# Performance work log

Hardware: AMD Instinct MI355X
Metric: run time of the kernel (lower is better)

Reference implementation:

```python
import jax, jax.numpy as jnp
import numpy as np

THR = 1.0        # snntorch Leaky default threshold
SLOPE = 25.0     # fast_sigmoid default slope
NUM_STEPS = 15
BETAS = (0.9, 0.88, 0.86, 0.84, 0.82)

@jax.custom_vjp
def fire(mem):
    # Heaviside forward, fast_sigmoid surrogate backward
    return (mem > THR).astype(mem.dtype)

def _fire_fwd(mem):
    return fire(mem), mem

def _fire_bwd(mem, g):
    return (g / (SLOPE * jnp.abs(mem - THR) + 1.0) ** 2,)

fire.defvjp(_fire_fwd, _fire_bwd)

def lif(cur, mem, beta):
    # snntorch Leaky, reset_mechanism='subtract': reset computed from PREVIOUS mem
    reset = jax.lax.stop_gradient((mem > THR).astype(cur.dtype))
    mem_new = beta * mem + cur - reset * THR
    spk = fire(mem_new)
    return spk, mem_new

def setup_inputs() -> dict:
    key = jax.random.key(0)
    ks = jax.random.split(key, 13)
    B = 16384
    dims = [(256, 6), (256, 256), (256, 256), (256, 256), (128, 256), (3, 128)]
    inp = {"x": jax.random.normal(ks[0], (B, 6), dtype=jnp.float32)}
    for i, (o, fin) in enumerate(dims):
        s = 1.0 / np.sqrt(fin)
        inp[f"W{i+1}"] = jax.random.uniform(ks[1 + 2 * i], (o, fin), jnp.float32, -s, s)
        inp[f"b{i+1}"] = jax.random.uniform(ks[2 + 2 * i], (o,), jnp.float32, -s, s)
    return inp

def reference(x, W1, b1, W2, b2, W3, b3, W4, b4, W5, b5, W6, b6):
    B = x.shape[0]
    cur1 = x @ W1.T + b1  # input is constant across timesteps
    mems0 = (jnp.zeros((B, 256), x.dtype), jnp.zeros((B, 256), x.dtype),
             jnp.zeros((B, 256), x.dtype), jnp.zeros((B, 256), x.dtype),
             jnp.zeros((B, 128), x.dtype))

    def step(carry, _):
        (m1, m2, m3, m4, m5), acc = carry
        spk1, m1 = lif(cur1, m1, BETAS[0])
        spk2, m2 = lif(spk1 @ W2.T + b2, m2, BETAS[1])
        spk3, m3 = lif(spk2 @ W3.T + b3, m3, BETAS[2])
        spk4, m4 = lif(spk3 @ W4.T + b4, m4, BETAS[3])
        spk5, m5 = lif(spk4 @ W5.T + b5, m5, BETAS[4])
        out = spk5 @ W6.T + b6
        return ((m1, m2, m3, m4, m5), acc + out), None

    (_, out_sum), _ = jax.lax.scan(step, (mems0, jnp.zeros((B, 3), x.dtype)),
                                   None, length=NUM_STEPS)
    return out_sum / NUM_STEPS
```

## Files before the change

kernel.cpp:

```cpp
#include <hip/hip_runtime.h>

#define B_SZ 16384

__global__ __launch_bounds__(256) void k_transpose(const float* __restrict__ src,
                                                   float* __restrict__ dst,
                                                   int R, int C) {
    __shared__ float tile[32][33];
    int bx = blockIdx.x * 32, by = blockIdx.y * 32;
    int tx = threadIdx.x & 31, ty = threadIdx.x >> 5;
#pragma unroll
    for (int r = ty; r < 32; r += 8) {
        int gr = by + r, gc = bx + tx;
        if (gr < R && gc < C) tile[r][tx] = src[gr * C + gc];
    }
    __syncthreads();
#pragma unroll
    for (int r = ty; r < 32; r += 8) {
        int gr = bx + r, gc = by + tx;
        if (gr < C && gc < R) dst[gr * R + gc] = tile[tx][r];
    }
}

__device__ __forceinline__ void mm256(const float* __restrict__ WT,
                                      const float (*slds)[16],
                                      const int* flagrow, int q, int g0,
                                      float* acc) {
#pragma unroll
    for (int k = 0; k < 16; ++k) acc[k] = 0.f;
    int4 f = *(const int4*)flagrow;
    if ((f.x | f.y | f.z | f.w) == 0) return;
    const float4* wp = (const float4*)WT + q;
#pragma unroll 4
    for (int i = 0; i < 256; ++i) {
        float4 w4 = wp[i * 64];
        float4 s4 = *(const float4*)&slds[i][g0];
        acc[0]  = fmaf(s4.x, w4.x, acc[0]);
        acc[1]  = fmaf(s4.y, w4.x, acc[1]);
        acc[2]  = fmaf(s4.z, w4.x, acc[2]);
        acc[3]  = fmaf(s4.w, w4.x, acc[3]);
        acc[4]  = fmaf(s4.x, w4.y, acc[4]);
        acc[5]  = fmaf(s4.y, w4.y, acc[5]);
        acc[6]  = fmaf(s4.z, w4.y, acc[6]);
        acc[7]  = fmaf(s4.w, w4.y, acc[7]);
        acc[8]  = fmaf(s4.x, w4.z, acc[8]);
        acc[9]  = fmaf(s4.y, w4.z, acc[9]);
        acc[10] = fmaf(s4.z, w4.z, acc[10]);
        acc[11] = fmaf(s4.w, w4.z, acc[11]);
        acc[12] = fmaf(s4.x, w4.w, acc[12]);
        acc[13] = fmaf(s4.y, w4.w, acc[13]);
        acc[14] = fmaf(s4.z, w4.w, acc[14]);
        acc[15] = fmaf(s4.w, w4.w, acc[15]);
    }
}

__device__ __forceinline__ int lif4x4(float* m, const float* acc, const float* b4,
                                      float beta, float (*slds)[16], int j0, int g0) {
    int any = 0;
#pragma unroll
    for (int jj = 0; jj < 4; ++jj) {
        float4 sp;
#pragma unroll
        for (int gg = 0; gg < 4; ++gg) {
            int k = jj * 4 + gg;
            float cur = acc[k] + b4[jj];
            float mp  = m[k];
            float mn  = fmaf(beta, mp, cur) - (mp > 1.f ? 1.f : 0.f);
            m[k] = mn;
            int s1 = (mn > 1.f);
            any |= s1;
            ((float*)&sp)[gg] = s1 ? 1.f : 0.f;
        }
        *(float4*)&slds[j0 + jj][g0] = sp;
    }
    return any;
}

__global__ __launch_bounds__(256, 3) void k_snn(
    const float* __restrict__ x,   const float* __restrict__ W1, const float* __restrict__ b1,
    const float* __restrict__ Wt2, const float* __restrict__ b2,
    const float* __restrict__ Wt3, const float* __restrict__ b3,
    const float* __restrict__ Wt4, const float* __restrict__ b4,
    const float* __restrict__ Wt5, const float* __restrict__ b5,
    const float* __restrict__ W6,  const float* __restrict__ b6,
    float* __restrict__ out)
{
    __shared__ __align__(16) float slds[256][16];
    __shared__ float w6l[3][128];
    __shared__ float xl[16][8];
    __shared__ __align__(16) int flags[5][4];

    const int t    = threadIdx.x;
    const int s0   = blockIdx.x * 16;
    const int q    = t >> 2, r = t & 3;
    const int j0   = q * 4, g0 = r * 4;
    const int lane = t & 63, wvid = t >> 6;

    for (int k = t; k < 384; k += 256) ((float*)w6l)[k] = W6[k];
    if (t < 128) { int g = t >> 3, c = t & 7; xl[g][c] = (c < 6) ? x[(s0 + g) * 6 + c] : 0.f; }
    __syncthreads();

    const float4 b2q = *(const float4*)&b2[j0];
    const float4 b3q = *(const float4*)&b3[j0];
    const float4 b4q = *(const float4*)&b4[j0];
    const float2 b5q = *(const float2*)&b5[q * 2];
    const int og = t / 3, ok = t - og * 3;
    const float b6v = (t < 48) ? b6[ok] : 0.f;

    float cur1[16];
#pragma unroll
    for (int jj = 0; jj < 4; ++jj) {
        float w1r[6];
#pragma unroll
        for (int k = 0; k < 6; ++k) w1r[k] = W1[(j0 + jj) * 6 + k];
        float bb = b1[j0 + jj];
#pragma unroll
        for (int gg = 0; gg < 4; ++gg) {
            float s = 0.f;
#pragma unroll
            for (int k = 0; k < 6; ++k) s = fmaf(xl[g0 + gg][k], w1r[k], s);
            cur1[jj * 4 + gg] = s + bb;
        }
    }

    float m1[16], m2[16], m3[16], m4[16], m5[8], acc[16];
#pragma unroll
    for (int k = 0; k < 16; ++k) { m1[k] = 0.f; m2[k] = 0.f; m3[k] = 0.f; m4[k] = 0.f; }
#pragma unroll
    for (int k = 0; k < 8; ++k) m5[k] = 0.f;
    float accout = 0.f;
    const float zb[4] = {0.f, 0.f, 0.f, 0.f};

#pragma unroll 1
    for (int step = 0; step < 15; ++step) {
        __syncthreads();

        {
            int any = lif4x4(m1, cur1, zb, 0.9f, slds, j0, g0);
            unsigned long long bl = __ballot(any);
            if (lane == 0) flags[0][wvid] = (bl != 0ULL) ? 1 : 0;
        }
        __syncthreads();

        mm256(Wt2, slds, &flags[0][0], q, g0, acc);
        __syncthreads();
        {
            int any = lif4x4(m2, acc, (const float*)&b2q, 0.88f, slds, j0, g0);
            unsigned long long bl = __ballot(any);
            if (lane == 0) flags[1][wvid] = (bl != 0ULL) ? 1 : 0;
        }
        __syncthreads();

        mm256(Wt3, slds, &flags[1][0], q, g0, acc);
        __syncthreads();
        {
            int any = lif4x4(m3, acc, (const float*)&b3q, 0.86f, slds, j0, g0);
            unsigned long long bl = __ballot(any);
            if (lane == 0) flags[2][wvid] = (bl != 0ULL) ? 1 : 0;
        }
        __syncthreads();

        mm256(Wt4, slds, &flags[2][0], q, g0, acc);
        __syncthreads();
        {
            int any = lif4x4(m4, acc, (const float*)&b4q, 0.84f, slds, j0, g0);
            unsigned long long bl = __ballot(any);
            if (lane == 0) flags[3][wvid] = (bl != 0ULL) ? 1 : 0;
        }
        __syncthreads();

        {
            float acc5[8];
#pragma unroll
            for (int k = 0; k < 8; ++k) acc5[k] = 0.f;
            int4 f = *(const int4*)&flags[3][0];
            if (f.x | f.y | f.z | f.w) {
                const float2* wp5 = (const float2*)Wt5 + q;
#pragma unroll 4
                for (int i = 0; i < 256; ++i) {
                    float2 w2 = wp5[i * 64];
                    float4 s4 = *(const float4*)&slds[i][g0];
                    acc5[0] = fmaf(s4.x, w2.x, acc5[0]);
                    acc5[1] = fmaf(s4.y, w2.x, acc5[1]);
                    acc5[2] = fmaf(s4.z, w2.x, acc5[2]);
                    acc5[3] = fmaf(s4.w, w2.x, acc5[3]);
                    acc5[4] = fmaf(s4.x, w2.y, acc5[4]);
                    acc5[5] = fmaf(s4.y, w2.y, acc5[5]);
                    acc5[6] = fmaf(s4.z, w2.y, acc5[6]);
                    acc5[7] = fmaf(s4.w, w2.y, acc5[7]);
                }
            }
            __syncthreads();
            int any = 0;
#pragma unroll
            for (int jj = 0; jj < 2; ++jj) {
                float4 sp;
#pragma unroll
                for (int gg = 0; gg < 4; ++gg) {
                    int k = jj * 4 + gg;
                    float cur = acc5[k] + ((const float*)&b5q)[jj];
                    float mp  = m5[k];
                    float mn  = fmaf(0.82f, mp, cur) - (mp > 1.f ? 1.f : 0.f);
                    m5[k] = mn;
                    int s1 = (mn > 1.f);
                    any |= s1;
                    ((float*)&sp)[gg] = s1 ? 1.f : 0.f;
                }
                *(float4*)&slds[q * 2 + jj][g0] = sp;
            }
            unsigned long long bl = __ballot(any);
            if (lane == 0) flags[4][wvid] = (bl != 0ULL) ? 1 : 0;
        }
        __syncthreads();

        {
            int4 f = *(const int4*)&flags[4][0];
            if (t < 48) {
                float ov = b6v;
                if (f.x | f.y | f.z | f.w) {
                    float s = 0.f;
#pragma unroll 4
                    for (int i = 0; i < 128; ++i) s = fmaf(slds[i][og], w6l[ok][i], s);
                    ov = s + b6v;
                }
                accout += ov;
            }
        }
    }

    if (t < 48) out[(s0 + og) * 3 + ok] = accout / 15.0f;
}

extern "C" void kernel_launch(void* const* d_in, const int* in_sizes, int n_in,
                              void* d_out, int out_size, void* d_ws, size_t ws_size,
                              hipStream_t stream) {
    const float* x  = (const float*)d_in[0];
    const float* W1 = (const float*)d_in[1];
    const float* b1 = (const float*)d_in[2];
    const float* W2 = (const float*)d_in[3];
    const float* b2 = (const float*)d_in[4];
    const float* W3 = (const float*)d_in[5];
    const float* b3 = (const float*)d_in[6];
    const float* W4 = (const float*)d_in[7];
    const float* b4 = (const float*)d_in[8];
    const float* W5 = (const float*)d_in[9];
    const float* b5 = (const float*)d_in[10];
    const float* W6 = (const float*)d_in[11];
    const float* b6 = (const float*)d_in[12];
    float* out = (float*)d_out;

    float* ws  = (float*)d_ws;
    float* Wt2 = ws;
    float* Wt3 = Wt2 + 65536;
    float* Wt4 = Wt3 + 65536;
    float* Wt5 = Wt4 + 65536;
    size_t need = (size_t)(65536 * 3 + 32768) * sizeof(float);
    if (ws_size < need) return;

    k_transpose<<<dim3(8, 8), 256, 0, stream>>>(W2, Wt2, 256, 256);
    k_transpose<<<dim3(8, 8), 256, 0, stream>>>(W3, Wt3, 256, 256);
    k_transpose<<<dim3(8, 8), 256, 0, stream>>>(W4, Wt4, 256, 256);
    k_transpose<<<dim3(8, 4), 256, 0, stream>>>(W5, Wt5, 128, 256);
    k_snn<<<B_SZ / 16, 256, 0, stream>>>(x, W1, b1, Wt2, b2, Wt3, b3,
                                         Wt4, b4, Wt5, b5, W6, b6, out);
}
```

Measured before the change: 2.640 ms.

## Ping-pong spike buffers to drop barriers and retile to 8 neurons x 2 samples

Spikes now go into two alternating LDS buffers, so each layer writes one buffer while the next matmul reads the other. This removes the barrier that separated each matmul from the following LIF write, leaving about five block syncs per timestep instead of eleven. Each thread now computes 8 output neurons for 2 samples instead of 4 for 4. Weights are read as two float4s per row across paired input rows, against a k-pair interleaved spike layout. The cost is double the spike LDS footprint and more complex indexing, which may change bank-conflict behaviour and register pressure.

```diff
diff --git a/kernel.cpp b/kernel.cpp
--- a/kernel.cpp
+++ b/kernel.cpp
@@ -21,56 +21,119 @@
     }
 }
 
-__device__ __forceinline__ void mm256(const float* __restrict__ WT,
-                                      const float (*slds)[16],
-                                      const int* flagrow, int q, int g0,
-                                      float* acc) {
+
+__device__ __forceinline__ void mm256_8x2(const float* __restrict__ WT,
+                                          const float (*sp)[16][2],
+                                          const int* flagrow, int q, int r,
+                                          float* acc) {
 #pragma unroll
     for (int k = 0; k < 16; ++k) acc[k] = 0.f;
     int4 f = *(const int4*)flagrow;
     if ((f.x | f.y | f.z | f.w) == 0) return;
-    const float4* wp = (const float4*)WT + q;
-#pragma unroll 4
-    for (int i = 0; i < 256; ++i) {
-        float4 w4 = wp[i * 64];
-        float4 s4 = *(const float4*)&slds[i][g0];
-        acc[0]  = fmaf(s4.x, w4.x, acc[0]);
-        acc[1]  = fmaf(s4.y, w4.x, acc[1]);
-        acc[2]  = fmaf(s4.z, w4.x, acc[2]);
-        acc[3]  = fmaf(s4.w, w4.x, acc[3]);
-        acc[4]  = fmaf(s4.x, w4.y, acc[4]);
-        acc[5]  = fmaf(s4.y, w4.y, acc[5]);
-        acc[6]  = fmaf(s4.z, w4.y, acc[6]);
-        acc[7]  = fmaf(s4.w, w4.y, acc[7]);
-        acc[8]  = fmaf(s4.x, w4.z, acc[8]);
-        acc[9]  = fmaf(s4.y, w4.z, acc[9]);
-        acc[10] = fmaf(s4.z, w4.z, acc[10]);
-        acc[11] = fmaf(s4.w, w4.z, acc[11]);
-        acc[12] = fmaf(s4.x, w4.w, acc[12]);
-        acc[13] = fmaf(s4.y, w4.w, acc[13]);
-        acc[14] = fmaf(s4.z, w4.w, acc[14]);
-        acc[15] = fmaf(s4.w, w4.w, acc[15]);
-    }
-}
-
-__device__ __forceinline__ int lif4x4(float* m, const float* acc, const float* b4,
-                                      float beta, float (*slds)[16], int j0, int g0) {
+#pragma unroll 2
+    for (int ip = 0; ip < 128; ++ip) {
+        float4 s4 = *(const float4*)&sp[ip][r * 2][0];
+        const float* w0 = WT + (2 * ip) * 256 + q * 8;
+        float4 wa0 = *(const float4*)(w0);
+        float4 wa1 = *(const float4*)(w0 + 4);
+        float4 wb0 = *(const float4*)(w0 + 256);
+        float4 wb1 = *(const float4*)(w0 + 260);
+        acc[0]  = fmaf(s4.x, wa0.x, acc[0]);  acc[0]  = fmaf(s4.y, wb0.x, acc[0]);
+        acc[1]  = fmaf(s4.z, wa0.x, acc[1]);  acc[1]  = fmaf(s4.w, wb0.x, acc[1]);
+        acc[2]  = fmaf(s4.x, wa0.y, acc[2]);  acc[2]  = fmaf(s4.y, wb0.y, acc[2]);
+        acc[3]  = fmaf(s4.z, wa0.y, acc[3]);  acc[3]  = fmaf(s4.w, wb0.y, acc[3]);
+        acc[4]  = fmaf(s4.x, wa0.z, acc[4]);  acc[4]  = fmaf(s4.y, wb0.z, acc[4]);
+        acc[5]  = fmaf(s4.z, wa0.z, acc[5]);  acc[5]  = fmaf(s4.w, wb0.z, acc[5]);
+        acc[6]  = fmaf(s4.x, wa0.w, acc[6]);  acc[6]  = fmaf(s4.y, wb0.w, acc[6]);
+        acc[7]  = fmaf(s4.z, wa0.w, acc[7]);  acc[7]  = fmaf(s4.w, wb0.w, acc[7]);
+        acc[8]  = fmaf(s4.x, wa1.x, acc[8]);  acc[8]  = fmaf(s4.y, wb1.x, acc[8]);
+        acc[9]  = fmaf(s4.z, wa1.x, acc[9]);  acc[9]  = fmaf(s4.w, wb1.x, acc[9]);
+        acc[10] = fmaf(s4.x, wa1.y, acc[10]); acc[10] = fmaf(s4.y, wb1.y, acc[10]);
+        acc[11] = fmaf(s4.z, wa1.y, acc[11]); acc[11] = fmaf(s4.w, wb1.y, acc[11]);
+        acc[12] = fmaf(s4.x, wa1.z, acc[12]); acc[12] = fmaf(s4.y, wb1.z, acc[12]);
+        acc[13] = fmaf(s4.z, wa1.z, acc[13]); acc[13] = fmaf(s4.w, wb1.z, acc[13]);
+        acc[14] = fmaf(s4.x, wa1.w, acc[14]); acc[14] = fmaf(s4.y, wb1.w, acc[14]);
+        acc[15] = fmaf(s4.z, wa1.w, acc[15]); acc[15] = fmaf(s4.w, wb1.w, acc[15]);
+    }
+}
+
+__device__ __forceinline__ void mm128_4x2(const float* __restrict__ WT5,
+                                          const float (*sp)[16][2],
+                                          const int* flagrow, int q, int r,
+                                          float* acc) {
+#pragma unroll
+    for (int k = 0; k < 8; ++k) acc[k] = 0.f;
+    int4 f = *(const int4*)flagrow;
+    if ((f.x | f.y | f.z | f.w) == 0) return;
+#pragma unroll 2
+    for (int ip = 0; ip < 128; ++ip) {
+        float4 s4 = *(const float4*)&sp[ip][r * 2][0];
+        const float* w0 = WT5 + (2 * ip) * 128 + q * 4;
+        float4 wa = *(const float4*)(w0);
+        float4 wb = *(const float4*)(w0 + 128);
+        acc[0] = fmaf(s4.x, wa.x, acc[0]); acc[0] = fmaf(s4.y, wb.x, acc[0]);
+        acc[1] = fmaf(s4.z, wa.x, acc[1]); acc[1] = fmaf(s4.w, wb.x, acc[1]);
+        acc[2] = fmaf(s4.x, wa.y, acc[2]); acc[2] = fmaf(s4.y, wb.y, acc[2]);
+        acc[3] = fmaf(s4.z, wa.y, acc[3]); acc[3] = fmaf(s4.w, wb.y, acc[3]);
+        acc[4] = fmaf(s4.x, wa.z, acc[4]); acc[4] = fmaf(s4.y, wb.z, acc[4]);
+        acc[5] = fmaf(s4.z, wa.z, acc[5]); acc[5] = fmaf(s4.w, wb.z, acc[5]);
+        acc[6] = fmaf(s4.x, wa.w, acc[6]); acc[6] = fmaf(s4.y, wb.w, acc[6]);
+        acc[7] = fmaf(s4.z, wa.w, acc[7]); acc[7] = fmaf(s4.w, wb.w, acc[7]);
+    }
+}
+
+__device__ __forceinline__ int lif8x2(float* m, const float* acc, const float* b8,
+                                      float beta, float (*sp)[16][2], int j0, int g0) {
     int any = 0;
 #pragma unroll
-    for (int jj = 0; jj < 4; ++jj) {
-        float4 sp;
-#pragma unroll
-        for (int gg = 0; gg < 4; ++gg) {
-            int k = jj * 4 + gg;
-            float cur = acc[k] + b4[jj];
-            float mp  = m[k];
-            float mn  = fmaf(beta, mp, cur) - (mp > 1.f ? 1.f : 0.f);
-            m[k] = mn;
-            int s1 = (mn > 1.f);
-            any |= s1;
-            ((float*)&sp)[gg] = s1 ? 1.f : 0.f;
+    for (int k2 = 0; k2 < 4; ++k2) {
+        float2 spA, spB;
+#pragma unroll
+        for (int e = 0; e < 2; ++e) {
+            int jj = 2 * k2 + e;
+#pragma unroll
+            for (int gg = 0; gg < 2; ++gg) {
+                int k = jj * 2 + gg;
+                float cur = acc[k] + b8[jj];
+                float mp  = m[k];
+                float mn  = fmaf(beta, mp, cur) - (mp > 1.f ? 1.f : 0.f);
+                m[k] = mn;
+                int s1 = (mn > 1.f);
+                any |= s1;
+                float sv = s1 ? 1.f : 0.f;
+                if (gg == 0) ((float*)&spA)[e] = sv; else ((float*)&spB)[e] = sv;
+            }
         }
-        *(float4*)&slds[j0 + jj][g0] = sp;
+        *(float2*)&sp[(j0 >> 1) + k2][g0][0]     = spA;
+        *(float2*)&sp[(j0 >> 1) + k2][g0 + 1][0] = spB;
+    }
+    return any;
+}
+
+__device__ __forceinline__ int lif4x2(float* m, const float* acc, const float* b4v,
+                                      float (*sp)[16][2], int j05, int g0) {
+    int any = 0;
+#pragma unroll
+    for (int k2 = 0; k2 < 2; ++k2) {
+        float2 spA, spB;
+#pragma unroll
+        for (int e = 0; e < 2; ++e) {
+            int jj = 2 * k2 + e;
+#pragma unroll
+            for (int gg = 0; gg < 2; ++gg) {
+                int k = jj * 2 + gg;
+                float cur = acc[k] + b4v[jj];
+                float mp  = m[k];
+                float mn  = fmaf(0.82f, mp, cur) - (mp > 1.f ? 1.f : 0.f);
+                m[k] = mn;
+                int s1 = (mn > 1.f);
+                any |= s1;
+                float sv = s1 ? 1.f : 0.f;
+                if (gg == 0) ((float*)&spA)[e] = sv; else ((float*)&spB)[e] = sv;
+            }
+        }
+        *(float2*)&sp[(j05 >> 1) + k2][g0][0]     = spA;
+        *(float2*)&sp[(j05 >> 1) + k2][g0 + 1][0] = spB;
     }
     return any;
 }
@@ -84,41 +147,46 @@
     const float* __restrict__ W6,  const float* __restrict__ b6,
     float* __restrict__ out)
 {
-    __shared__ __align__(16) float slds[256][16];
+    __shared__ __align__(16) float sppA[128][16][2];
+    __shared__ __align__(16) float sppB[128][16][2];
     __shared__ float w6l[3][128];
     __shared__ float xl[16][8];
     __shared__ __align__(16) int flags[5][4];
 
     const int t    = threadIdx.x;
     const int s0   = blockIdx.x * 16;
-    const int q    = t >> 2, r = t & 3;
-    const int j0   = q * 4, g0 = r * 4;
+    const int q    = t >> 3;
+    const int r    = t & 7;
+    const int j0   = q * 8;
+    const int j05  = q * 4;
+    const int g0   = r * 2;
     const int lane = t & 63, wvid = t >> 6;
 
     for (int k = t; k < 384; k += 256) ((float*)w6l)[k] = W6[k];
     if (t < 128) { int g = t >> 3, c = t & 7; xl[g][c] = (c < 6) ? x[(s0 + g) * 6 + c] : 0.f; }
     __syncthreads();
 
-    const float4 b2q = *(const float4*)&b2[j0];
-    const float4 b3q = *(const float4*)&b3[j0];
-    const float4 b4q = *(const float4*)&b4[j0];
-    const float2 b5q = *(const float2*)&b5[q * 2];
+    float b2r[8], b3r[8], b4r[8], b5r[4];
+    *(float4*)&b2r[0] = *(const float4*)&b2[j0]; *(float4*)&b2r[4] = *(const float4*)&b2[j0 + 4];
+    *(float4*)&b3r[0] = *(const float4*)&b3[j0]; *(float4*)&b3r[4] = *(const float4*)&b3[j0 + 4];
+    *(float4*)&b4r[0] = *(const float4*)&b4[j0]; *(float4*)&b4r[4] = *(const float4*)&b4[j0 + 4];
+    *(float4*)&b5r[0] = *(const float4*)&b5[j05];
     const int og = t / 3, ok = t - og * 3;
     const float b6v = (t < 48) ? b6[ok] : 0.f;
 
     float cur1[16];
 #pragma unroll
-    for (int jj = 0; jj < 4; ++jj) {
+    for (int jj = 0; jj < 8; ++jj) {
         float w1r[6];
 #pragma unroll
         for (int k = 0; k < 6; ++k) w1r[k] = W1[(j0 + jj) * 6 + k];
         float bb = b1[j0 + jj];
 #pragma unroll
-        for (int gg = 0; gg < 4; ++gg) {
+        for (int gg = 0; gg < 2; ++gg) {
             float s = 0.f;
 #pragma unroll
             for (int k = 0; k < 6; ++k) s = fmaf(xl[g0 + gg][k], w1r[k], s);
-            cur1[jj * 4 + gg] = s + bb;
+            cur1[jj * 2 + gg] = s + bb;
         }
     }
 
@@ -128,104 +196,47 @@
 #pragma unroll
     for (int k = 0; k < 8; ++k) m5[k] = 0.f;
     float accout = 0.f;
-    const float zb[4] = {0.f, 0.f, 0.f, 0.f};
+    const float zb8[8] = {0.f,0.f,0.f,0.f,0.f,0.f,0.f,0.f};
+
+#define SETFLAG(L) { unsigned long long bl = __ballot(any); if (lane == 0) flags[L][wvid] = (bl != 0ULL) ? 1 : 0; }
+
+#define STEP(SX, SY)                                                            \
+    { int any = lif8x2(m1, cur1, zb8, 0.9f, SX, j0, g0); SETFLAG(0); }          \
+    __syncthreads();                                                            \
+    mm256_8x2(Wt2, SX, &flags[0][0], q, r, acc);                                \
+    { int any = lif8x2(m2, acc, b2r, 0.88f, SY, j0, g0); SETFLAG(1); }          \
+    __syncthreads();                                                            \
+    mm256_8x2(Wt3, SY, &flags[1][0], q, r, acc);                                \
+    { int any = lif8x2(m3, acc, b3r, 0.86f, SX, j0, g0); SETFLAG(2); }          \
+    __syncthreads();                                                            \
+    mm256_8x2(Wt4, SX, &flags[2][0], q, r, acc);                                \
+    { int any = lif8x2(m4, acc, b4r, 0.84f, SY, j0, g0); SETFLAG(3); }          \
+    __syncthreads();                                                            \
+    mm128_4x2(Wt5, SY, &flags[3][0], q, r, acc);                                \
+    { int any = lif4x2(m5, acc, b5r, SX, j05, g0); SETFLAG(4); }                \
+    __syncthreads();                                                            \
+    { int4 f = *(const int4*)&flags[4][0];                                      \
+      if (t < 48) {                                                             \
+          float s = 0.f;                                                        \
+          if (f.x | f.y | f.z | f.w) {                                          \
+              _Pragma("unroll 4")                                               \
+              for (int ip = 0; ip < 64; ++ip) {                                 \
+                  float2 sv = *(const float2*)&SX[ip][og][0];                   \
+                  s = fmaf(sv.x, w6l[ok][2 * ip], s);                           \
+                  s = fmaf(sv.y, w6l[ok][2 * ip + 1], s);                       \
+              }                                                                 \
+          }                                                                     \
+          accout += s + b6v;                                                    \
+      } }
 
 #pragma unroll 1
-    for (int step = 0; step < 15; ++step) {
-        __syncthreads();
-
-        {
-            int any = lif4x4(m1, cur1, zb, 0.9f, slds, j0, g0);
-            unsigned long long bl = __ballot(any);
-            if (lane == 0) flags[0][wvid] = (bl != 0ULL) ? 1 : 0;
-        }
-        __syncthreads();
-
-        mm256(Wt2, slds, &flags[0][0], q, g0, acc);
-        __syncthreads();
-        {
-            int any = lif4x4(m2, acc, (const float*)&b2q, 0.88f, slds, j0, g0);
-            unsigned long long bl = __ballot(any);
-            if (lane == 0) flags[1][wvid] = (bl != 0ULL) ? 1 : 0;
-        }
-        __syncthreads();
-
-        mm256(Wt3, slds, &flags[1][0], q, g0, acc);
-        __syncthreads();
-        {
-            int any = lif4x4(m3, acc, (const float*)&b3q, 0.86f, slds, j0, g0);
-            unsigned long long bl = __ballot(any);
-            if (lane == 0) flags[2][wvid] = (bl != 0ULL) ? 1 : 0;
-        }
-        __syncthreads();
-
-        mm256(Wt4, slds, &flags[2][0], q, g0, acc);
-        __syncthreads();
-        {
-            int any = lif4x4(m4, acc, (const float*)&b4q, 0.84f, slds, j0, g0);
-            unsigned long long bl = __ballot(any);
-            if (lane == 0) flags[3][wvid] = (bl != 0ULL) ? 1 : 0;
-        }
-        __syncthreads();
-
-        {
-            float acc5[8];
-#pragma unroll
-            for (int k = 0; k < 8; ++k) acc5[k] = 0.f;
-            int4 f = *(const int4*)&flags[3][0];
-            if (f.x | f.y | f.z | f.w) {
-                const float2* wp5 = (const float2*)Wt5 + q;
-#pragma unroll 4
-                for (int i = 0; i < 256; ++i) {
-                    float2 w2 = wp5[i * 64];
-                    float4 s4 = *(const float4*)&slds[i][g0];
-                    acc5[0] = fmaf(s4.x, w2.x, acc5[0]);
-                    acc5[1] = fmaf(s4.y, w2.x, acc5[1]);
-                    acc5[2] = fmaf(s4.z, w2.x, acc5[2]);
-                    acc5[3] = fmaf(s4.w, w2.x, acc5[3]);
-                    acc5[4] = fmaf(s4.x, w2.y, acc5[4]);
-                    acc5[5] = fmaf(s4.y, w2.y, acc5[5]);
-                    acc5[6] = fmaf(s4.z, w2.y, acc5[6]);
-                    acc5[7] = fmaf(s4.w, w2.y, acc5[7]);
-                }
-            }
-            __syncthreads();
-            int any = 0;
-#pragma unroll
-            for (int jj = 0; jj < 2; ++jj) {
-                float4 sp;
-#pragma unroll
-                for (int gg = 0; gg < 4; ++gg) {
-                    int k = jj * 4 + gg;
-                    float cur = acc5[k] + ((const float*)&b5q)[jj];
-                    float mp  = m5[k];
-                    float mn  = fmaf(0.82f, mp, cur) - (mp > 1.f ? 1.f : 0.f);
-                    m5[k] = mn;
-                    int s1 = (mn > 1.f);
-                    any |= s1;
-                    ((float*)&sp)[gg] = s1 ? 1.f : 0.f;
-                }
-                *(float4*)&slds[q * 2 + jj][g0] = sp;
-            }
-            unsigned long long bl = __ballot(any);
-            if (lane == 0) flags[4][wvid] = (bl != 0ULL) ? 1 : 0;
-        }
-        __syncthreads();
-
-        {
-            int4 f = *(const int4*)&flags[4][0];
-            if (t < 48) {
-                float ov = b6v;
-                if (f.x | f.y | f.z | f.w) {
-                    float s = 0.f;
-#pragma unroll 4
-                    for (int i = 0; i < 128; ++i) s = fmaf(slds[i][og], w6l[ok][i], s);
-                    ov = s + b6v;
-                }
-                accout += ov;
-            }
-        }
-    }
+    for (int s2 = 0; s2 < 7; ++s2) {
+        STEP(sppA, sppB)
+        STEP(sppB, sppA)
+    }
+    STEP(sppA, sppB)
+#undef STEP
+#undef SETFLAG
 
     if (t < 48) out[(s0 + og) * 3 + ok] = accout / 15.0f;
 }
```

After: 3.674 ms. 1.39x slower.
